# Kernel optimization log

Hardware: AMD Instinct MI355X
Metric: run time of the kernel (lower is better)

The kernel has to match this reference:

```python
import jax, jax.numpy as jnp
import numpy as np

N = 200000      # nodes
E = 1600000     # directed edges (before self-loops)
G = 5000        # graphs (molecules)
IN, HID, OUT, HEADS = 128, 128, 128, 3


def gat_layer(x, src, dst, W, a_src, a_dst, b, heads, out_dim, concat):
    n = x.shape[0]
    h = (x @ W).reshape(n, heads, out_dim)                 # [N,H,F]
    al_s = jnp.einsum('nhf,hf->nh', h, a_src)              # [N,H]
    al_d = jnp.einsum('nhf,hf->nh', h, a_dst)
    e = jax.nn.leaky_relu(al_s[src] + al_d[dst], 0.2)      # [E,H]
    m = jax.ops.segment_max(e, dst, num_segments=n)        # softmax over incoming edges
    ex = jnp.exp(e - m[dst])
    den = jax.ops.segment_sum(ex, dst, num_segments=n)
    alpha = ex / (den[dst] + 1e-16)                        # [E,H]
    msg = h[src] * alpha[..., None]                        # [E,H,F]
    agg = jax.ops.segment_sum(msg, dst, num_segments=n)    # [N,H,F]
    agg = agg.reshape(n, heads * out_dim) if concat else agg.mean(axis=1)
    return agg + b


def setup_inputs() -> dict:
    key = jax.random.key(0)
    ks = jax.random.split(key, 16)
    d = {}
    d['x'] = jax.random.normal(ks[0], (N, IN), dtype=jnp.float32)
    d['edge_index'] = jax.random.randint(ks[1], (2, E), 0, N, dtype=jnp.int64)
    d['batch'] = jnp.sort(jax.random.randint(ks[2], (N,), 0, G, dtype=jnp.int64))
    s = 0.1
    d['W1'] = jax.random.normal(ks[3], (IN, HEADS * HID), jnp.float32) * s
    d['a1s'] = jax.random.normal(ks[4], (HEADS, HID), jnp.float32) * s
    d['a1d'] = jax.random.normal(ks[5], (HEADS, HID), jnp.float32) * s
    d['b1'] = jnp.zeros((HEADS * HID,), jnp.float32)
    d['W2'] = jax.random.normal(ks[6], (HEADS * HID, HEADS * HID), jnp.float32) * s
    d['a2s'] = jax.random.normal(ks[7], (HEADS, HID), jnp.float32) * s
    d['a2d'] = jax.random.normal(ks[8], (HEADS, HID), jnp.float32) * s
    d['b2'] = jnp.zeros((HEADS * HID,), jnp.float32)
    d['W3'] = jax.random.normal(ks[9], (HEADS * HID, OUT), jnp.float32) * s
    d['a3s'] = jax.random.normal(ks[10], (1, OUT), jnp.float32) * s
    d['a3d'] = jax.random.normal(ks[11], (1, OUT), jnp.float32) * s
    d['b3'] = jnp.zeros((OUT,), jnp.float32)
    return d


def reference(x, edge_index, batch, W1, a1s, a1d, b1, W2, a2s, a2d, b2, W3, a3s, a3d, b3):
    # PyG GATConv default add_self_loops=True
    loops = jnp.arange(N, dtype=edge_index.dtype)
    src = jnp.concatenate([edge_index[0], loops])
    dst = jnp.concatenate([edge_index[1], loops])
    h = jax.nn.leaky_relu(gat_layer(x, src, dst, W1, a1s, a1d, b1, HEADS, HID, True), 0.2)
    h = jax.nn.leaky_relu(gat_layer(h, src, dst, W2, a2s, a2d, b2, HEADS, HID, True), 0.2)
    h = jax.nn.leaky_relu(gat_layer(h, src, dst, W3, a3s, a3d, b3, 1, OUT, False), 0.2)
    # global mean pool over graphs
    sums = jax.ops.segment_sum(h, batch, num_segments=G)            # [G,OUT]
    cnt = jax.ops.segment_sum(jnp.ones((N,), h.dtype), batch, num_segments=G)
    return sums / jnp.maximum(cnt, 1.0)[:, None]
```

## Files before the change

### kernel.cpp

```cpp
#include <hip/hip_runtime.h>
#include <hip/hip_bf16.h>
#include <math.h>

#define LRELU_SLOPE 0.2f
typedef __hip_bfloat16 bf16;
typedef __hip_bfloat162 bf16x2;

typedef short s8v __attribute__((ext_vector_type(8)));
typedef short s4v __attribute__((ext_vector_type(4)));
typedef float f4v __attribute__((ext_vector_type(4)));
typedef int   i4v __attribute__((ext_vector_type(4)));
typedef unsigned int u4v __attribute__((ext_vector_type(4)));

__device__ __forceinline__ float lrelu(float v) { return v > 0.f ? v : LRELU_SLOPE * v; }
__device__ __forceinline__ float b2f(short b) {
  return __uint_as_float(((unsigned)(unsigned short)b) << 16);
}

__device__ __forceinline__ void st2(float* p, float x, float y) {
  *(float2*)p = float2{x, y};
}

__device__ __forceinline__ u4v make_srd(const void* p) {
  u4v r;
  unsigned long long a = (unsigned long long)p;
  r.x = (unsigned)a; r.y = (unsigned)(a >> 32);
  r.z = 0xFFFFFFFFu;
  r.w = 0x00020000u;
  return r;
}
__device__ __forceinline__ void bstore16_nt(u4v srd, int byteoff, i4v d) {
  asm volatile("buffer_store_dwordx4 %0, %1, %2, 0 offen sc1 nt"
               :: "v"(d), "v"(byteoff), "s"(srd));
}


__global__ void k_zero(unsigned int* __restrict__ p, long n) {
  long i = (long)blockIdx.x * blockDim.x + threadIdx.x;
  if (i < n) p[i] = 0u;
}

__global__ void k_zero_out(float* __restrict__ out, int n) {
  int i = blockIdx.x * blockDim.x + threadIdx.x;
  if (i < n) out[i] = 0.f;
}


__global__ void k_cvt(const float* __restrict__ x, bf16* __restrict__ xb, long n) {
  long i = (long)blockIdx.x * blockDim.x + threadIdx.x;
  if (i < n) xb[i] = __float2bfloat16(x[i]);
}

__global__ void k_tw2(const float* __restrict__ W, bf16* __restrict__ B2, int K, int NN) {
  int tid = blockIdx.x * blockDim.x + threadIdx.x;
  int total = (K * NN) >> 3;
  if (tid >= total) return;
  int f = tid >> 6, l = tid & 63;
  int nfr = NN >> 4;
  int k32 = f / nfr, ct = f - k32 * nfr;
  int col = ct * 16 + (l & 15);
  int krow = k32 * 32 + (l >> 4) * 8;
  s8v v;
#pragma unroll
  for (int j = 0; j < 8; ++j) {
    bf16 b = __float2bfloat16(W[(size_t)(krow + j) * NN + col]);
    v[j] = *(short*)&b;
  }
  *(s8v*)&B2[(size_t)tid * 8] = v;
}


__global__ void k_hist(const int* __restrict__ dst, int* __restrict__ deg, int E, int Et) {
  int e = blockIdx.x * blockDim.x + threadIdx.x;
  if (e >= Et) return;
  int d = (e < E) ? dst[e] : (e - E);
  atomicAdd(&deg[d], 1);
}

__global__ void k_hist1(const int* __restrict__ idx, int* __restrict__ deg, int n) {
  int i = blockIdx.x * blockDim.x + threadIdx.x;
  if (i < n) atomicAdd(&deg[idx[i]], 1);
}

__global__ void k_scan1(const int* __restrict__ deg, int* __restrict__ offs,
                        int* __restrict__ bsum, int n) {
  __shared__ int sd[256];
  int t = threadIdx.x;
  int base = blockIdx.x * 1024 + t * 4;
  int v[4]; int tsum = 0;
#pragma unroll
  for (int i = 0; i < 4; ++i) { v[i] = (base + i < n) ? deg[base + i] : 0; tsum += v[i]; }
  sd[t] = tsum;
  __syncthreads();
  for (int off = 1; off < 256; off <<= 1) {
    int x = (t >= off) ? sd[t - off] : 0;
    __syncthreads();
    sd[t] += x;
    __syncthreads();
  }
  int excl = sd[t] - tsum;
#pragma unroll
  for (int i = 0; i < 4; ++i) { if (base + i < n) offs[base + i] = excl; excl += v[i]; }
  if (t == 255) bsum[blockIdx.x] = sd[255];
}

__global__ void k_scan2(int* bsum, int nb) {
  int t = threadIdx.x;
  if (nb > 256) {
    if (t == 0 && blockIdx.x == 0) {
      int run = 0;
      for (int i = 0; i < nb; ++i) { int x = bsum[i]; bsum[i] = run; run += x; }
    }
    return;
  }
  int v = (t < nb) ? bsum[t] : 0;
  int lane = t & 63, wv = t >> 6;
  int s = v;
#pragma unroll
  for (int off = 1; off < 64; off <<= 1) {
    int u = __shfl_up(s, off, 64);
    if (lane >= off) s += u;
  }
  __shared__ int wsum[4];
  if (lane == 63) wsum[wv] = s;
  __syncthreads();
  int add = 0;
  for (int w = 0; w < wv; ++w) add += wsum[w];
  if (t < nb) bsum[t] = add + s - v;
}

__global__ void k_scan3(int* __restrict__ offs, const int* __restrict__ bsum, int n, int total) {
  int t = threadIdx.x;
  int base = blockIdx.x * 1024 + t * 4;
  int add = bsum[blockIdx.x];
#pragma unroll
  for (int i = 0; i < 4; ++i) if (base + i < n) offs[base + i] += add;
  if (blockIdx.x == 0 && t == 0) offs[n] = total;
}

__global__ void k_scatter(const int* __restrict__ src, const int* __restrict__ dst,
                          const int* __restrict__ offs, int* __restrict__ cur,
                          int* __restrict__ ssrc, int E, int Et) {
  int e = blockIdx.x * blockDim.x + threadIdx.x;
  if (e >= Et) return;
  int s, d;
  if (e < E) { s = src[e]; d = dst[e]; } else { s = d = e - E; }
  int pos = offs[d] + atomicAdd(&cur[d], 1);
  ssrc[pos] = s;
}


template <int K, int NN>
__global__ __launch_bounds__(512, 4) void k_gemm_t(const bf16* __restrict__ A,
                                                   const bf16* __restrict__ B2,
                                                   bf16* __restrict__ C) {
  constexpr int nk = K / 32;
  constexpr int nfr = NN >> 4;
  __shared__ __align__(16) short sA[2][256 * 32];
  int t = threadIdx.x;
  int wv = t >> 6, lane = t & 63;
  int mg = wv >> 1, ng = wv & 1;
  int quad = lane >> 4, l15 = lane & 15;
  size_t bm0 = (size_t)blockIdx.x * 256;
  int ctb = blockIdx.y * 8 + ng * 4;

  int sr = t >> 2, p = t & 3;
  int c = p ^ (sr & 3);
  const bf16* g0 = A + (bm0 + sr) * (size_t)K + c * 8;
  const bf16* g1 = g0 + (size_t)128 * K;
  const bf16* Bp = B2 + ((size_t)ctb << 9) + lane * 8;

  f4v acc[4][4];
#pragma unroll
  for (int ms = 0; ms < 4; ++ms)
#pragma unroll
    for (int bn = 0; bn < 4; ++bn) acc[ms][bn] = f4v{0, 0, 0, 0};

#define STAGE(step, buf)                                                        \
  do {                                                                          \
    __builtin_amdgcn_global_load_lds(                                           \
        (const __attribute__((address_space(1))) void*)(g0 + (step) * 32),      \
        (__attribute__((address_space(3))) void*)((char*)sA[buf] + wv * 1024),  \
        16, 0, 0);                                                              \
    __builtin_amdgcn_global_load_lds(                                           \
        (const __attribute__((address_space(1))) void*)(g1 + (step) * 32),      \
        (__attribute__((address_space(3))) void*)((char*)sA[buf] + 8192 + wv * 1024), \
        16, 0, 0);                                                              \
  } while (0)

  STAGE(0, 0);
  __syncthreads();

  for (int ik = 0; ik < nk; ++ik) {
    int cur = ik & 1;
    if (ik + 1 < nk) STAGE(ik + 1, cur ^ 1);

    const char* sb = (const char*)sA[cur];
    s8v af[4];
#pragma unroll
    for (int ms = 0; ms < 4; ++ms) {
      int row = mg * 64 + ms * 16 + l15;
      int pos = quad ^ (row & 3);
      af[ms] = *(const s8v*)(sb + row * 64 + pos * 16);
    }
    s8v pb[4];
#pragma unroll
    for (int bn = 0; bn < 4; ++bn)
      pb[bn] = *(const s8v*)(Bp + ((size_t)(ik * nfr + bn) << 9));
#pragma unroll
    for (int ms = 0; ms < 4; ++ms)
#pragma unroll
      for (int bn = 0; bn < 4; ++bn)
        acc[ms][bn] = __builtin_amdgcn_mfma_f32_16x16x32_bf16(af[ms], pb[bn], acc[ms][bn], 0, 0, 0);

    __syncthreads();
  }
#undef STAGE

#pragma unroll
  for (int ms = 0; ms < 4; ++ms)
#pragma unroll
    for (int bn = 0; bn < 4; ++bn) {
      int coln = (ctb + bn) * 16 + l15;
      size_t rbase = bm0 + mg * 64 + ms * 16 + quad * 4;
#pragma unroll
      for (int r = 0; r < 4; ++r)
        C[(rbase + r) * NN + coln] = __float2bfloat16(acc[ms][bn][r]);
    }
}


template <int H>
__global__ void k_al(const bf16* __restrict__ h, const float* __restrict__ as,
                     const float* __restrict__ ad, float* __restrict__ al_s,
                     float* __restrict__ al_d, int N) {
  constexpr int SP = (H > 1) ? 4 : 1;
  int n = (blockIdx.x * blockDim.x + threadIdx.x) >> 6;
  int lane = threadIdx.x & 63;
  if (n >= N) return;
  int hd = lane >> 4;
  bool active = (hd < H);
  int hdc = active ? hd : 0;
  int f8 = (lane & 15) * 8;
  const bf16* hp = h + (size_t)n * (H * 128) + hdc * 128 + f8;
  s8v hv = *(const s8v*)hp;
  float ss = 0.f, sd = 0.f;
#pragma unroll
  for (int i = 0; i < 8; ++i) {
    float v = b2f(hv[i]);
    ss += v * as[hdc * 128 + f8 + i];
    sd += v * ad[hdc * 128 + f8 + i];
  }
#pragma unroll
  for (int off = 8; off; off >>= 1) {
    ss += __shfl_xor(ss, off, 64);
    sd += __shfl_xor(sd, off, 64);
  }
  if (active && (lane & 15) == 0) {
    al_s[n * SP + hd] = ss;
    al_d[n * SP + hd] = sd;
  }
}


template <int CPL> struct HVec;
template <> struct HVec<8> { typedef s8v T; };
template <> struct HVec<4> { typedef s4v T; };

template <int H, typename OT>
__global__ __launch_bounds__(256) void k_attn_agg(const bf16* __restrict__ hbuf,
                           const int* __restrict__ ssrc,
                           const int* __restrict__ offs, const float* __restrict__ al_s,
                           const float* __restrict__ al_d, const float* __restrict__ bias,
                           OT* __restrict__ out, int N) {
  constexpr int SW  = (H > 1) ? 4 : 2;
  constexpr int ROW = H * 128;
  constexpr int CPL = (H > 1) ? 8 : 4;
  constexpr int NL  = ROW / CPL;
  typedef typename HVec<CPL>::T hvec;

  __shared__ __align__(16) float stash[4][64 * SW];
  int n = (blockIdx.x * blockDim.x + threadIdx.x) >> 6;
  int lane = threadIdx.x & 63;
  if (n >= N) return;
  float* st = stash[threadIdx.x >> 6];
  int start = offs[n], end = offs[n + 1];

  float ald[H];
  if constexpr (H > 1) {
    float4 t = *(const float4*)&al_d[(size_t)n * 4];
    ald[0] = t.x; ald[1] = t.y; ald[2] = t.z;
  } else {
    ald[0] = al_d[n];
  }

  bool act = lane < NL;
  int c0 = act ? lane * CPL : 0;
  int hd_l = c0 >> 7;

  float m[H];
  float den = 0.f;
  float acc[CPL];
#pragma unroll
  for (int hd = 0; hd < H; ++hd) m[hd] = -1e30f;
#pragma unroll
  for (int i = 0; i < CPL; ++i) acc[i] = 0.f;

  for (int cb = start; cb < end; cb += 64) {
    int cl = end - cb; if (cl > 64) cl = 64;
    bool el = lane < cl;
    int mys = el ? ssrc[cb + lane] : 0;
    float ev[H];
    if constexpr (H > 1) {
      float4 av = *(const float4*)&al_s[(size_t)mys * 4];
      ev[0] = av.x; ev[1] = av.y; ev[2] = av.z;
    } else {
      ev[0] = al_s[mys];
    }
#pragma unroll
    for (int hd = 0; hd < H; ++hd)
      ev[hd] = el ? lrelu(ev[hd] + ald[hd]) : -1e30f;

    float nm[H];
#pragma unroll
    for (int hd = 0; hd < H; ++hd) {
      float v = ev[hd];
#pragma unroll
      for (int off = 32; off; off >>= 1) v = fmaxf(v, __shfl_xor(v, off, 64));
      nm[hd] = fmaxf(v, m[hd]);
    }
    if (cb > start) {
      float sc[H];
#pragma unroll
      for (int hd = 0; hd < H; ++hd) sc[hd] = __expf(m[hd] - nm[hd]);
      float so = sc[hd_l];
      den *= so;
#pragma unroll
      for (int i = 0; i < CPL; ++i) acc[i] *= so;
    }
#pragma unroll
    for (int hd = 0; hd < H; ++hd) m[hd] = nm[hd];

    float myex[H];
#pragma unroll
    for (int hd = 0; hd < H; ++hd) myex[hd] = el ? __expf(ev[hd] - m[hd]) : 0.f;

    __builtin_amdgcn_wave_barrier();
    if constexpr (H > 1) {
      float4 s4{__int_as_float(mys), myex[0], myex[1], myex[2]};
      *(float4*)&st[lane * 4] = s4;
    } else {
      float2 s2{__int_as_float(mys), myex[0]};
      *(float2*)&st[lane * 2] = s2;
    }
    asm volatile("s_waitcnt lgkmcnt(0)" ::: "memory");
    __builtin_amdgcn_wave_barrier();

    for (int r = 0; r < cl; r += 8) {
      int su[8]; float a[8];
#pragma unroll
      for (int u = 0; u < 8; ++u) {
        if constexpr (H > 1) {
          float4 ed = *(const float4*)&st[(r + u) * 4];
          su[u] = __float_as_int(ed.x);
          a[u] = (hd_l == 0) ? ed.y : ((hd_l == 1) ? ed.z : ed.w);
        } else {
          float2 ed = *(const float2*)&st[(r + u) * 2];
          su[u] = __float_as_int(ed.x);
          a[u] = ed.y;
        }
        den += a[u];
      }
      hvec hv[8];
#pragma unroll
      for (int u = 0; u < 8; ++u)
        hv[u] = *(const hvec*)(hbuf + (size_t)su[u] * ROW + c0);
#pragma unroll
      for (int u = 0; u < 8; ++u)
#pragma unroll
        for (int i = 0; i < CPL; ++i)
          acc[i] += a[u] * b2f(hv[u][i]);
    }
  }

  if (act) {
    float rr = 1.f / (den + 1e-16f);
    u4v srd = make_srd(out);
    int boff = (int)(((size_t)n * ROW + c0) * sizeof(OT));
    if constexpr (sizeof(OT) == 2) {
      union { s8v s; i4v i; } u;
#pragma unroll
      for (int i = 0; i < CPL; ++i) {
        float o = lrelu(acc[i] * rr + bias[c0 + i]);
        bf16 b = __float2bfloat16(o);
        u.s[i] = *(short*)&b;
      }
      bstore16_nt(srd, boff, u.i);
    } else {
      union { float4 f; i4v i; } u;
      u.f.x = lrelu(acc[0] * rr + bias[c0 + 0]);
      u.f.y = lrelu(acc[1] * rr + bias[c0 + 1]);
      u.f.z = lrelu(acc[2] * rr + bias[c0 + 2]);
      u.f.w = lrelu(acc[3] * rr + bias[c0 + 3]);
      bstore16_nt(srd, boff, u.i);
    }
  }
}


__global__ void k_pool(const float* __restrict__ h, const int* __restrict__ goffs,
                       float* __restrict__ out, int G) {
  int g = (blockIdx.x * blockDim.x + threadIdx.x) >> 6;
  int lane = threadIdx.x & 63;
  if (g >= G) return;
  int s = goffs[g], e = goffs[g + 1];
  float ax = 0.f, ay = 0.f;
  for (int n = s; n < e; ++n) {
    float2 v = *(const float2*)&h[(size_t)n * 128 + lane * 2];
    ax += v.x; ay += v.y;
  }
  float c = fmaxf((float)(e - s), 1.f);
  st2(&out[(size_t)g * 128 + lane * 2], ax / c, ay / c);
}


extern "C" void kernel_launch(void* const* d_in, const int* in_sizes, int n_in,
                              void* d_out, int out_size, void* d_ws, size_t ws_size,
                              hipStream_t stream) {
  const float* x   = (const float*)d_in[0];
  const int*   ei  = (const int*)d_in[1];
  const int*   bat = (const int*)d_in[2];
  const float* W1  = (const float*)d_in[3];
  const float* a1s = (const float*)d_in[4];
  const float* a1d = (const float*)d_in[5];
  const float* b1  = (const float*)d_in[6];
  const float* W2  = (const float*)d_in[7];
  const float* a2s = (const float*)d_in[8];
  const float* a2d = (const float*)d_in[9];
  const float* b2  = (const float*)d_in[10];
  const float* W3  = (const float*)d_in[11];
  const float* a3s = (const float*)d_in[12];
  const float* a3d = (const float*)d_in[13];
  const float* b3  = (const float*)d_in[14];
  float* out = (float*)d_out;

  const int N = in_sizes[2];
  const int E = in_sizes[1] / 2;
  const int Et = E + N;
  const int G = out_size / 128;

  const int MB = (N + 255) / 256;
  const int Mpad = MB * 256;

  char* p = (char*)d_ws;
  auto carve = [&](size_t bytes) { void* r = (void*)p; p += (bytes + 255) & ~(size_t)255; return r; };
  bf16*  bufA   = (bf16*)carve((size_t)Mpad * 384 * 2);
  bf16*  bufB   = (bf16*)carve((size_t)Mpad * 384 * 2);
  float* al_s   = (float*)carve((size_t)N * 4 * 4);
  float* al_d   = (float*)carve((size_t)N * 4 * 4);
  int*   ssrc   = (int*)carve((size_t)Et * 4);
  int*   offs   = (int*)carve((size_t)(N + 1) * 4);
  int*   deg    = (int*)carve((size_t)N * 4);
  int*   cur    = (int*)carve((size_t)N * 4);
  int*   bsum   = (int*)carve(4096 * 4);
  int*   gdeg   = (int*)carve((size_t)G * 4);
  int*   goffs  = (int*)carve((size_t)(G + 1) * 4);
  bf16*  Wp1    = (bf16*)carve((size_t)384 * 128 * 2);
  bf16*  Wp2    = (bf16*)carve((size_t)384 * 384 * 2);
  bf16*  Wp3    = (bf16*)carve((size_t)128 * 384 * 2);
  size_t need = (size_t)(p - (char*)d_ws);

  if (ws_size < need) {
    k_zero_out<<<(out_size + 255) / 256, 256, 0, stream>>>(out, out_size);
    return;
  }

  const int* esrc = ei;
  const int* edst = ei + E;

  int ebl = (Et + 255) / 256;
  int NB = (N + 1023) / 1024;
  int GB = (G + 1023) / 1024;
  int nodeWaveBlocks = (N * 64 + 255) / 256;

  bf16* xb = bufA;
  k_cvt<<<((long)N * 128 + 255) / 256, 256, 0, stream>>>(x, xb, (long)N * 128);
  k_tw2<<<(128 * 384 / 8 + 255) / 256, 256, 0, stream>>>(W1, Wp1, 128, 384);
  k_tw2<<<(384 * 384 / 8 + 255) / 256, 256, 0, stream>>>(W2, Wp2, 384, 384);
  k_tw2<<<(384 * 128 / 8 + 255) / 256, 256, 0, stream>>>(W3, Wp3, 384, 128);

  k_zero<<<(N + 255) / 256, 256, 0, stream>>>((unsigned int*)deg, N);
  k_hist<<<ebl, 256, 0, stream>>>(edst, deg, E, Et);
  k_scan1<<<NB, 256, 0, stream>>>(deg, offs, bsum, N);
  k_scan2<<<1, 256, 0, stream>>>(bsum, NB);
  k_scan3<<<NB, 256, 0, stream>>>(offs, bsum, N, Et);
  k_zero<<<(N + 255) / 256, 256, 0, stream>>>((unsigned int*)cur, N);
  k_scatter<<<ebl, 256, 0, stream>>>(esrc, edst, offs, cur, ssrc, E, Et);

  k_zero<<<(G + 255) / 256, 256, 0, stream>>>((unsigned int*)gdeg, G);
  k_hist1<<<(N + 255) / 256, 256, 0, stream>>>(bat, gdeg, N);
  k_scan1<<<GB, 256, 0, stream>>>(gdeg, goffs, bsum, G);
  k_scan2<<<1, 256, 0, stream>>>(bsum, GB);
  k_scan3<<<GB, 256, 0, stream>>>(goffs, bsum, G, N);

  k_gemm_t<128, 384><<<dim3(MB, 3), 512, 0, stream>>>(xb, Wp1, bufB);
  k_al<3><<<nodeWaveBlocks, 256, 0, stream>>>(bufB, a1s, a1d, al_s, al_d, N);
  k_attn_agg<3, bf16><<<nodeWaveBlocks, 256, 0, stream>>>(bufB, ssrc, offs, al_s, al_d, b1, bufA, N);

  k_gemm_t<384, 384><<<dim3(MB, 3), 512, 0, stream>>>(bufA, Wp2, bufB);
  k_al<3><<<nodeWaveBlocks, 256, 0, stream>>>(bufB, a2s, a2d, al_s, al_d, N);
  k_attn_agg<3, bf16><<<nodeWaveBlocks, 256, 0, stream>>>(bufB, ssrc, offs, al_s, al_d, b2, bufA, N);

  k_gemm_t<384, 128><<<dim3(MB, 1), 512, 0, stream>>>(bufA, Wp3, bufB);
  k_al<1><<<nodeWaveBlocks, 256, 0, stream>>>(bufB, a3s, a3d, al_s, al_d, N);
  float* out3 = (float*)bufA;
  k_attn_agg<1, float><<<nodeWaveBlocks, 256, 0, stream>>>(bufB, ssrc, offs, al_s, al_d, b3, out3, N);

  k_pool<<<(G * 64 + 255) / 256, 256, 0, stream>>>(out3, goffs, out, G);
}
```

Baseline: 1.399 ms.

## Fuse attention logit dot-products into GEMM epilogue and vectorize input conversion

```diff
diff --git a/kernel.cpp b/kernel.cpp
--- a/kernel.cpp
+++ b/kernel.cpp
@@ -46,9 +46,22 @@
 }
 
 
-__global__ void k_cvt(const float* __restrict__ x, bf16* __restrict__ xb, long n) {
+__global__ void k_cvt(const float* __restrict__ x, bf16* __restrict__ xb, long n8) {
   long i = (long)blockIdx.x * blockDim.x + threadIdx.x;
-  if (i < n) xb[i] = __float2bfloat16(x[i]);
+  if (i >= n8) return;
+  const float4* xp = (const float4*)(x + i * 8);
+  float4 a = xp[0], b = xp[1];
+  s8v v;
+  bf16 t;
+  t = __float2bfloat16(a.x); v[0] = *(short*)&t;
+  t = __float2bfloat16(a.y); v[1] = *(short*)&t;
+  t = __float2bfloat16(a.z); v[2] = *(short*)&t;
+  t = __float2bfloat16(a.w); v[3] = *(short*)&t;
+  t = __float2bfloat16(b.x); v[4] = *(short*)&t;
+  t = __float2bfloat16(b.y); v[5] = *(short*)&t;
+  t = __float2bfloat16(b.z); v[6] = *(short*)&t;
+  t = __float2bfloat16(b.w); v[7] = *(short*)&t;
+  *(s8v*)&xb[i * 8] = v;
 }
 
 __global__ void k_tw2(const float* __restrict__ W, bf16* __restrict__ B2, int K, int NN) {
@@ -153,15 +166,22 @@
 template <int K, int NN>
 __global__ __launch_bounds__(512, 4) void k_gemm_t(const bf16* __restrict__ A,
                                                    const bf16* __restrict__ B2,
-                                                   bf16* __restrict__ C) {
+                                                   bf16* __restrict__ C,
+                                                   const float* __restrict__ as_,
+                                                   const float* __restrict__ ad_,
+                                                   float* __restrict__ al_s,
+                                                   float* __restrict__ al_d,
+                                                   int N) {
   constexpr int nk = K / 32;
   constexpr int nfr = NN >> 4;
+  constexpr int SP = (NN == 384) ? 4 : 1;
   __shared__ __align__(16) short sA[2][256 * 32];
   int t = threadIdx.x;
   int wv = t >> 6, lane = t & 63;
   int mg = wv >> 1, ng = wv & 1;
   int quad = lane >> 4, l15 = lane & 15;
   size_t bm0 = (size_t)blockIdx.x * 256;
+  int hd = (NN == 384) ? blockIdx.y : 0;
   int ctb = blockIdx.y * 8 + ng * 4;
 
   int sr = t >> 2, p = t & 3;
@@ -217,48 +237,39 @@
   }
 #undef STAGE
 
-#pragma unroll
-  for (int ms = 0; ms < 4; ++ms)
-#pragma unroll
-    for (int bn = 0; bn < 4; ++bn) {
-      int coln = (ctb + bn) * 16 + l15;
-      size_t rbase = bm0 + mg * 64 + ms * 16 + quad * 4;
-#pragma unroll
-      for (int r = 0; r < 4; ++r)
-        C[(rbase + r) * NN + coln] = __float2bfloat16(acc[ms][bn][r]);
-    }
-}
-
-
-template <int H>
-__global__ void k_al(const bf16* __restrict__ h, const float* __restrict__ as,
-                     const float* __restrict__ ad, float* __restrict__ al_s,
-                     float* __restrict__ al_d, int N) {
-  constexpr int SP = (H > 1) ? 4 : 1;
-  int n = (blockIdx.x * blockDim.x + threadIdx.x) >> 6;
-  int lane = threadIdx.x & 63;
-  if (n >= N) return;
-  int hd = lane >> 4;
-  bool active = (hd < H);
-  int hdc = active ? hd : 0;
-  int f8 = (lane & 15) * 8;
-  const bf16* hp = h + (size_t)n * (H * 128) + hdc * 128 + f8;
-  s8v hv = *(const s8v*)hp;
-  float ss = 0.f, sd = 0.f;
-#pragma unroll
-  for (int i = 0; i < 8; ++i) {
-    float v = b2f(hv[i]);
-    ss += v * as[hdc * 128 + f8 + i];
-    sd += v * ad[hdc * 128 + f8 + i];
-  }
-#pragma unroll
-  for (int off = 8; off; off >>= 1) {
-    ss += __shfl_xor(ss, off, 64);
-    sd += __shfl_xor(sd, off, 64);
-  }
-  if (active && (lane & 15) == 0) {
-    al_s[n * SP + hd] = ss;
-    al_d[n * SP + hd] = sd;
+  float asv[4], adv[4];
+#pragma unroll
+  for (int bn = 0; bn < 4; ++bn) {
+    int cwh = (ng * 4 + bn) * 16 + l15;
+    asv[bn] = as_[hd * 128 + cwh];
+    adv[bn] = ad_[hd * 128 + cwh];
+  }
+
+#pragma unroll
+  for (int ms = 0; ms < 4; ++ms) {
+#pragma unroll
+    for (int r = 0; r < 4; ++r) {
+      size_t rown = bm0 + mg * 64 + ms * 16 + quad * 4 + r;
+      float ps = 0.f, pd = 0.f;
+#pragma unroll
+      for (int bn = 0; bn < 4; ++bn) {
+        int coln = (ctb + bn) * 16 + l15;
+        bf16 b = __float2bfloat16(acc[ms][bn][r]);
+        C[rown * NN + coln] = b;
+        float hv = b2f(*(short*)&b);
+        ps += hv * asv[bn];
+        pd += hv * adv[bn];
+      }
+#pragma unroll
+      for (int off = 1; off <= 8; off <<= 1) {
+        ps += __shfl_xor(ps, off, 64);
+        pd += __shfl_xor(pd, off, 64);
+      }
+      if (l15 == 0 && rown < (size_t)N) {
+        atomicAdd(&al_s[rown * SP + hd], ps);
+        atomicAdd(&al_d[rown * SP + hd], pd);
+      }
+    }
   }
 }
 
@@ -482,9 +493,11 @@
   int NB = (N + 1023) / 1024;
   int GB = (G + 1023) / 1024;
   int nodeWaveBlocks = (N * 64 + 255) / 256;
+  long alWords = (long)N * 8;
+  int alBlocks = (int)((alWords + 255) / 256);
 
   bf16* xb = bufA;
-  k_cvt<<<((long)N * 128 + 255) / 256, 256, 0, stream>>>(x, xb, (long)N * 128);
+  k_cvt<<<((long)N * 128 / 8 + 255) / 256, 256, 0, stream>>>(x, xb, (long)N * 128 / 8);
   k_tw2<<<(128 * 384 / 8 + 255) / 256, 256, 0, stream>>>(W1, Wp1, 128, 384);
   k_tw2<<<(384 * 384 / 8 + 255) / 256, 256, 0, stream>>>(W2, Wp2, 384, 384);
   k_tw2<<<(384 * 128 / 8 + 255) / 256, 256, 0, stream>>>(W3, Wp3, 384, 128);
@@ -503,16 +516,16 @@
   k_scan2<<<1, 256, 0, stream>>>(bsum, GB);
   k_scan3<<<GB, 256, 0, stream>>>(goffs, bsum, G, N);
 
-  k_gemm_t<128, 384><<<dim3(MB, 3), 512, 0, stream>>>(xb, Wp1, bufB);
-  k_al<3><<<nodeWaveBlocks, 256, 0, stream>>>(bufB, a1s, a1d, al_s, al_d, N);
+  k_zero<<<alBlocks, 256, 0, stream>>>((unsigned int*)al_s, alWords);
+  k_gemm_t<128, 384><<<dim3(MB, 3), 512, 0, stream>>>(xb, Wp1, bufB, a1s, a1d, al_s, al_d, N);
   k_attn_agg<3, bf16><<<nodeWaveBlocks, 256, 0, stream>>>(bufB, ssrc, offs, al_s, al_d, b1, bufA, N);
 
-  k_gemm_t<384, 384><<<dim3(MB, 3), 512, 0, stream>>>(bufA, Wp2, bufB);
-  k_al<3><<<nodeWaveBlocks, 256, 0, stream>>>(bufB, a2s, a2d, al_s, al_d, N);
+  k_zero<<<alBlocks, 256, 0, stream>>>((unsigned int*)al_s, alWords);
+  k_gemm_t<384, 384><<<dim3(MB, 3), 512, 0, stream>>>(bufA, Wp2, bufB, a2s, a2d, al_s, al_d, N);
   k_attn_agg<3, bf16><<<nodeWaveBlocks, 256, 0, stream>>>(bufB, ssrc, offs, al_s, al_d, b2, bufA, N);
 
-  k_gemm_t<384, 128><<<dim3(MB, 1), 512, 0, stream>>>(bufA, Wp3, bufB);
-  k_al<1><<<nodeWaveBlocks, 256, 0, stream>>>(bufB, a3s, a3d, al_s, al_d, N);
+  k_zero<<<alBlocks, 256, 0, stream>>>((unsigned int*)al_s, alWords);
+  k_gemm_t<384, 128><<<dim3(MB, 1), 512, 0, stream>>>(bufA, Wp3, bufB, a3s, a3d, al_s, al_d, N);
   float* out3 = (float*)bufA;
   k_attn_agg<1, float><<<nodeWaveBlocks, 256, 0, stream>>>(bufB, ssrc, offs, al_s, al_d, b3, out3, N);
 
```

Measured after the change: 1.474 ms. 1.05x slower.
